# Kernel tuning notes

Hardware: AMD Instinct MI355X
Metric: run time of the kernel (lower is better)

Reference implementation:

```python
import jax, jax.numpy as jnp
import numpy as np

N_NODES = 50000
N_EDGES = 800000
IN_DIM = 128
HID = 128
BN_EPS = 1e-5


def _linear_init(key, fan_in, fan_out):
    kw, kb = jax.random.split(key)
    bound = 1.0 / np.sqrt(fan_in)
    w = jax.random.uniform(kw, (fan_in, fan_out), minval=-bound, maxval=bound, dtype=jnp.float32)
    b = jax.random.uniform(kb, (fan_out,), minval=-bound, maxval=bound, dtype=jnp.float32)
    return w, b


def setup_inputs() -> dict:
    key = jax.random.key(0)
    ks = jax.random.split(key, 8)
    x = jax.random.normal(ks[0], (N_NODES, IN_DIM), dtype=jnp.float32)
    edge_index = jax.random.randint(ks[1], (2, N_EDGES), 0, N_NODES, dtype=jnp.int32)
    # GIN layer 0 MLP: Linear(IN_DIM,HID) -> ReLU -> Linear(HID,HID)
    w0a, b0a = _linear_init(ks[2], IN_DIM, HID)
    w0b, b0b = _linear_init(ks[3], HID, HID)
    # GIN layer 1 MLP
    w1a, b1a = _linear_init(ks[4], HID, HID)
    w1b, b1b = _linear_init(ks[5], HID, HID)
    # encoder BatchNorm affine params (torch init: gamma=1, beta=0)
    bn_gamma = jnp.ones((HID,), jnp.float32)
    bn_beta = jnp.zeros((HID,), jnp.float32)
    # projection head: Linear(HID,HID) -> BatchNorm -> PReLU -> Dropout
    pw, pb = _linear_init(ks[6], HID, HID)
    pbn_gamma = jnp.ones((HID,), jnp.float32)
    pbn_beta = jnp.zeros((HID,), jnp.float32)
    prelu_a = jnp.asarray(0.25, jnp.float32)  # torch PReLU default init
    return {
        'x': x, 'edge_index': edge_index,
        'w0a': w0a, 'b0a': b0a, 'w0b': w0b, 'b0b': b0b,
        'w1a': w1a, 'b1a': b1a, 'w1b': w1b, 'b1b': b1b,
        'bn_gamma': bn_gamma, 'bn_beta': bn_beta,
        'pw': pw, 'pb': pb, 'pbn_gamma': pbn_gamma, 'pbn_beta': pbn_beta,
        'prelu_a': prelu_a,
    }


def _batch_norm(x, gamma, beta):
    # training-mode BatchNorm1d: biased variance over the node (batch) dim
    mu = jnp.mean(x, axis=0)
    var = jnp.var(x, axis=0)
    return gamma * (x - mu) * jax.lax.rsqrt(var + BN_EPS) + beta


def _gin_conv(z, src, dst, wa, ba, wb, bb):
    # sum-aggregate neighbor features: out[i] = (1+eps)*z[i] + sum_{j->i} z[j], eps=0
    agg = jax.ops.segment_sum(z[src], dst, num_segments=N_NODES)
    h = z + agg
    h = jax.nn.relu(h @ wa + ba)
    return h @ wb + bb


def reference(x, edge_index, w0a, b0a, w0b, b0b, w1a, b1a, w1b, b1b,
              bn_gamma, bn_beta, pw, pb, pbn_gamma, pbn_beta, prelu_a):
    src, dst = edge_index[0], edge_index[1]
    z = x
    z = jax.nn.relu(_gin_conv(z, src, dst, w0a, b0a, w0b, b0b))  # dropout: identity (deterministic)
    z = jax.nn.relu(_gin_conv(z, src, dst, w1a, b1a, w1b, b1b))
    z = _batch_norm(z, bn_gamma, bn_beta)
    p = z @ pw + pb
    p = _batch_norm(p, pbn_gamma, pbn_beta)
    p = jnp.where(p > 0, p, prelu_a * p)  # PReLU, single shared parameter
    return z, p
```

## Files before the change

kernel.cpp:

```cpp
#include <hip/hip_runtime.h>
#include <hip/hip_bf16.h>

#define NN 50000
#define NE 800000
#define HD 128
#define BN_EPS 1e-5f
#define MSTR 132
#define NBUK 782
#define PB 200
#define CHUNK 4000

typedef __attribute__((ext_vector_type(8))) __bf16 bf16x8;
typedef __attribute__((ext_vector_type(4))) __bf16 bf16x4;
typedef __attribute__((ext_vector_type(4))) float floatx4;

__global__ __launch_bounds__(256) void k_cast(const float* __restrict__ X,
                                              __bf16* __restrict__ Y,
                                              int* __restrict__ gbtot) {
    const int t = blockIdx.x * 256 + threadIdx.x;
    if (t < 800) gbtot[t] = 0;
    const int i8 = t * 8;
    const float4 a = *(const float4*)&X[i8];
    const float4 b = *(const float4*)&X[i8 + 4];
    bf16x8 o;
    o[0] = (__bf16)a.x; o[1] = (__bf16)a.y; o[2] = (__bf16)a.z; o[3] = (__bf16)a.w;
    o[4] = (__bf16)b.x; o[5] = (__bf16)b.y; o[6] = (__bf16)b.z; o[7] = (__bf16)b.w;
    *(bf16x8*)&Y[i8] = o;
}

__global__ void k_wprep(const float* __restrict__ W0, const float* __restrict__ W1,
                        const float* __restrict__ W2, const float* __restrict__ W3,
                        const float* __restrict__ W4,
                        __bf16* __restrict__ Bh, __bf16* __restrict__ Bl) {
    const int n = blockIdx.x, m = blockIdx.y, k = threadIdx.x;
    const float* W = (m == 0) ? W0 : (m == 1) ? W1 : (m == 2) ? W2 : (m == 3) ? W3 : W4;
    const float w = W[k * HD + n];
    const __bf16 h = (__bf16)w;
    const int ct = n >> 4, lm = n & 15;
    const int ks = k >> 5, lq = (k & 31) >> 3, j = k & 7;
    const int lane = lq * 16 + lm;
    const size_t o = (size_t)m * HD * HD + (size_t)(((ct * 4 + ks) * 64) + lane) * 8 + j;
    Bh[o] = h;
    Bl[o] = (__bf16)(w - (float)h);
}

__global__ __launch_bounds__(256) void k_bcount(const int* __restrict__ dst,
                                                int* __restrict__ gbtot) {
    __shared__ int h[NBUK];
    for (int i = threadIdx.x; i < NBUK; i += 256) h[i] = 0;
    __syncthreads();
    const int e0 = blockIdx.x * CHUNK;
    for (int i = threadIdx.x; i < CHUNK; i += 256)
        atomicAdd(&h[dst[e0 + i] >> 6], 1);
    __syncthreads();
    for (int i = threadIdx.x; i < NBUK; i += 256) {
        const int v = h[i];
        if (v) atomicAdd(&gbtot[i], v);
    }
}

__global__ __launch_bounds__(256) void k_bscan(const int* __restrict__ gbtot,
                                               int* __restrict__ bbase,
                                               int* __restrict__ gcur,
                                               int* __restrict__ rowptr) {
    __shared__ int sh[256];
    const int t = threadIdx.x;
    int v[4];
    int s = 0;
#pragma unroll
    for (int j = 0; j < 4; ++j) {
        const int idx = t * 4 + j;
        v[j] = (idx < NBUK) ? gbtot[idx] : 0;
        s += v[j];
    }
    sh[t] = s;
    __syncthreads();
#pragma unroll
    for (int st = 1; st < 256; st <<= 1) {
        int add = (t >= st) ? sh[t - st] : 0;
        __syncthreads();
        sh[t] += add;
        __syncthreads();
    }
    int run = sh[t] - s;
#pragma unroll
    for (int j = 0; j < 4; ++j) {
        const int idx = t * 4 + j;
        if (idx < NBUK) { bbase[idx] = run; gcur[idx] = run; }
        run += v[j];
    }
    if (t == 255) bbase[NBUK] = run;
    if (t == 0) rowptr[NN] = NE;
}

__global__ __launch_bounds__(256) void k_bscatter(const int* __restrict__ src,
                                                  const int* __restrict__ dst,
                                                  int* __restrict__ gcur,
                                                  int2* __restrict__ pairs) {
    __shared__ int h[NBUK];
    __shared__ int cur[NBUK];
    for (int i = threadIdx.x; i < NBUK; i += 256) h[i] = 0;
    __syncthreads();
    const int e0 = blockIdx.x * CHUNK;
    for (int i = threadIdx.x; i < CHUNK; i += 256)
        atomicAdd(&h[dst[e0 + i] >> 6], 1);
    __syncthreads();
    for (int i = threadIdx.x; i < NBUK; i += 256) {
        const int v = h[i];
        if (v) cur[i] = atomicAdd(&gcur[i], v);
    }
    __syncthreads();
    for (int i = threadIdx.x; i < CHUNK; i += 256) {
        const int d = dst[e0 + i];
        const int pos = atomicAdd(&cur[d >> 6], 1);
        pairs[pos] = make_int2(src[e0 + i], d);
    }
}

__global__ __launch_bounds__(256) void k_csrfin(const int2* __restrict__ pairs,
                                                const int* __restrict__ bbase,
                                                int* __restrict__ rowptr,
                                                int* __restrict__ esrc) {
    __shared__ int cnt[64], lof[64], cur[64];
    const int b = blockIdx.x;
    const int s = bbase[b], e = bbase[b + 1];
    const int tid = threadIdx.x;
    if (tid < 64) cnt[tid] = 0;
    __syncthreads();
    for (int i = s + tid; i < e; i += 256)
        atomicAdd(&cnt[pairs[i].y & 63], 1);
    __syncthreads();
    if (tid == 0) {
        int r = 0;
#pragma unroll
        for (int j = 0; j < 64; ++j) { lof[j] = r; cur[j] = r; r += cnt[j]; }
    }
    __syncthreads();
    if (tid < 64) {
        const int node = b * 64 + tid;
        if (node < NN) rowptr[node] = s + lof[tid];
    }
    for (int i = s + tid; i < e; i += 256) {
        const int2 p = pairs[i];
        const int pos = atomicAdd(&cur[p.y & 63], 1);
        esrc[s + pos] = p.x;
    }
}

__device__ __forceinline__ void split8(const float4 a, const float4 b,
                                       bf16x8& hi, bf16x8& lo) {
    hi[0] = (__bf16)a.x; lo[0] = (__bf16)(a.x - (float)hi[0]);
    hi[1] = (__bf16)a.y; lo[1] = (__bf16)(a.y - (float)hi[1]);
    hi[2] = (__bf16)a.z; lo[2] = (__bf16)(a.z - (float)hi[2]);
    hi[3] = (__bf16)a.w; lo[3] = (__bf16)(a.w - (float)hi[3]);
    hi[4] = (__bf16)b.x; lo[4] = (__bf16)(b.x - (float)hi[4]);
    hi[5] = (__bf16)b.y; lo[5] = (__bf16)(b.y - (float)hi[5]);
    hi[6] = (__bf16)b.z; lo[6] = (__bf16)(b.z - (float)hi[6]);
    hi[7] = (__bf16)b.w; lo[7] = (__bf16)(b.w - (float)hi[7]);
}

__device__ __forceinline__ void addb8(float4& a, float4& b, const bf16x8 v) {
    a.x += (float)v[0]; a.y += (float)v[1]; a.z += (float)v[2]; a.w += (float)v[3];
    b.x += (float)v[4]; b.y += (float)v[5]; b.z += (float)v[6]; b.w += (float)v[7];
}

__global__ __launch_bounds__(256) void k_aggb(const __bf16* __restrict__ Z,
                                              const int* __restrict__ rowptr,
                                              const int* __restrict__ esrc,
                                              float* __restrict__ H) {
    const int g = threadIdx.x >> 4;
    const int lg = threadIdx.x & 15;
    const int node = blockIdx.x * 16 + g;
    const int cb = lg * 8;
    const int start = rowptr[node], end = rowptr[node + 1];
    float4 a = {0.f, 0.f, 0.f, 0.f}, b = {0.f, 0.f, 0.f, 0.f};
    addb8(a, b, *(const bf16x8*)&Z[(size_t)node * HD + cb]);
    int k = start;
    for (; k + 8 <= end; k += 8) {
        const int s0 = esrc[k + 0], s1 = esrc[k + 1];
        const int s2 = esrc[k + 2], s3 = esrc[k + 3];
        const int s4 = esrc[k + 4], s5 = esrc[k + 5];
        const int s6 = esrc[k + 6], s7 = esrc[k + 7];
        const bf16x8 v0 = *(const bf16x8*)&Z[(size_t)s0 * HD + cb];
        const bf16x8 v1 = *(const bf16x8*)&Z[(size_t)s1 * HD + cb];
        const bf16x8 v2 = *(const bf16x8*)&Z[(size_t)s2 * HD + cb];
        const bf16x8 v3 = *(const bf16x8*)&Z[(size_t)s3 * HD + cb];
        const bf16x8 v4 = *(const bf16x8*)&Z[(size_t)s4 * HD + cb];
        const bf16x8 v5 = *(const bf16x8*)&Z[(size_t)s5 * HD + cb];
        const bf16x8 v6 = *(const bf16x8*)&Z[(size_t)s6 * HD + cb];
        const bf16x8 v7 = *(const bf16x8*)&Z[(size_t)s7 * HD + cb];
        addb8(a, b, v0); addb8(a, b, v1); addb8(a, b, v2); addb8(a, b, v3);
        addb8(a, b, v4); addb8(a, b, v5); addb8(a, b, v6); addb8(a, b, v7);
    }
    for (; k + 4 <= end; k += 4) {
        const int s0 = esrc[k + 0], s1 = esrc[k + 1];
        const int s2 = esrc[k + 2], s3 = esrc[k + 3];
        const bf16x8 v0 = *(const bf16x8*)&Z[(size_t)s0 * HD + cb];
        const bf16x8 v1 = *(const bf16x8*)&Z[(size_t)s1 * HD + cb];
        const bf16x8 v2 = *(const bf16x8*)&Z[(size_t)s2 * HD + cb];
        const bf16x8 v3 = *(const bf16x8*)&Z[(size_t)s3 * HD + cb];
        addb8(a, b, v0); addb8(a, b, v1); addb8(a, b, v2); addb8(a, b, v3);
    }
    for (; k < end; ++k) {
        const int s = esrc[k];
        addb8(a, b, *(const bf16x8*)&Z[(size_t)s * HD + cb]);
    }
    *(float4*)&H[(size_t)node * HD + cb] = a;
    *(float4*)&H[(size_t)node * HD + cb + 4] = b;
}

__device__ __forceinline__ void mfma_pass(floatx4 (&acc)[8], const bf16x8 ah,
                                          const bf16x8 al, const __bf16* Bh,
                                          const __bf16* Bl, int ks, int lane) {
    bf16x8 bh[8], bl[8];
#pragma unroll
    for (int ct = 0; ct < 8; ++ct) {
        const size_t bo = (size_t)(((ct * 4 + ks) * 64) + lane) * 8;
        bh[ct] = *(const bf16x8*)&Bh[bo];
        bl[ct] = *(const bf16x8*)&Bl[bo];
    }
    __builtin_amdgcn_sched_barrier(0);
#pragma unroll
    for (int ct = 0; ct < 8; ++ct) {
        acc[ct] = __builtin_amdgcn_mfma_f32_16x16x32_bf16(al, bh[ct], acc[ct], 0, 0, 0);
        acc[ct] = __builtin_amdgcn_mfma_f32_16x16x32_bf16(ah, bl[ct], acc[ct], 0, 0, 0);
        acc[ct] = __builtin_amdgcn_mfma_f32_16x16x32_bf16(ah, bh[ct], acc[ct], 0, 0, 0);
    }
}

template <int STATS, int OUT16>
__global__ __launch_bounds__(256) void k_mlp(const float* __restrict__ A,
                                             const __bf16* __restrict__ Bh1,
                                             const __bf16* __restrict__ Bl1,
                                             const float* __restrict__ b1,
                                             const __bf16* __restrict__ Bh2,
                                             const __bf16* __restrict__ Bl2,
                                             const float* __restrict__ b2,
                                             float* __restrict__ C,
                                             __bf16* __restrict__ C16,
                                             float* __restrict__ pstat) {
    __shared__ float mid[4][16 * MSTR];
    __shared__ float ssum[128], ssq[128];
    const int tid = threadIdx.x;
    const int wid = tid >> 6, lane = tid & 63;
    const int lq = lane >> 4, lm = lane & 15;
    if (STATS) {
        if (tid < 128) { ssum[tid] = 0.f; ssq[tid] = 0.f; }
        __syncthreads();
    }
    const int rowbase = blockIdx.x * 64 + wid * 16;
    const int r0 = min(rowbase + lm, NN - 1);
    float* m = &mid[wid][0];

    bf16x8 ahv[4], alv[4];
    {
        float4 av[8];
#pragma unroll
        for (int ks = 0; ks < 4; ++ks) {
            const int kk = ks * 32 + lq * 8;
            av[ks * 2 + 0] = *(const float4*)&A[(size_t)r0 * HD + kk];
            av[ks * 2 + 1] = *(const float4*)&A[(size_t)r0 * HD + kk + 4];
        }
#pragma unroll
        for (int ks = 0; ks < 4; ++ks)
            split8(av[ks * 2], av[ks * 2 + 1], ahv[ks], alv[ks]);
    }
    floatx4 acc[8];
#pragma unroll
    for (int j = 0; j < 8; ++j) acc[j] = (floatx4){0.f, 0.f, 0.f, 0.f};
#pragma unroll
    for (int ks = 0; ks < 4; ++ks)
        mfma_pass(acc, ahv[ks], alv[ks], Bh1, Bl1, ks, lane);
#pragma unroll
    for (int ct = 0; ct < 8; ++ct) {
        const int col = ct * 16 + lm;
        const float bcol = b1[col];
#pragma unroll
        for (int r = 0; r < 4; ++r)
            m[(lq * 4 + r) * MSTR + col] = fmaxf(acc[ct][r] + bcol, 0.f);
    }
#pragma unroll
    for (int j = 0; j < 8; ++j) acc[j] = (floatx4){0.f, 0.f, 0.f, 0.f};
#pragma unroll
    for (int ks = 0; ks < 4; ++ks) {
        const int kk = ks * 32 + lq * 8;
        const float4 aa = *(const float4*)&m[lm * MSTR + kk];
        const float4 ab = *(const float4*)&m[lm * MSTR + kk + 4];
        bf16x8 ah, al;
        split8(aa, ab, ah, al);
        mfma_pass(acc, ah, al, Bh2, Bl2, ks, lane);
    }
#pragma unroll
    for (int ct = 0; ct < 8; ++ct) {
        const int col = ct * 16 + lm;
        const float bcol = b2[col];
#pragma unroll
        for (int r = 0; r < 4; ++r)
            m[(lq * 4 + r) * MSTR + col] = fmaxf(acc[ct][r] + bcol, 0.f);
    }
    float s0 = 0.f, s1 = 0.f, s2 = 0.f, s3 = 0.f;
    float q0 = 0.f, q1 = 0.f, q2 = 0.f, q3 = 0.f;
    const int c0 = (lane * 4) & 127;
#pragma unroll
    for (int p = 0; p < 8; ++p) {
        const int idx = p * 256 + lane * 4;
        const int r = idx >> 7;
        const float4 v = *(const float4*)&m[r * MSTR + c0];
        const int row = rowbase + r;
        if (row < NN) {
            if (OUT16) {
                bf16x4 o;
                o[0] = (__bf16)v.x; o[1] = (__bf16)v.y;
                o[2] = (__bf16)v.z; o[3] = (__bf16)v.w;
                *(bf16x4*)&C16[(size_t)row * HD + c0] = o;
            } else {
                *(float4*)&C[(size_t)row * HD + c0] = v;
            }
            if (STATS) {
                s0 += v.x; q0 = fmaf(v.x, v.x, q0);
                s1 += v.y; q1 = fmaf(v.y, v.y, q1);
                s2 += v.z; q2 = fmaf(v.z, v.z, q2);
                s3 += v.w; q3 = fmaf(v.w, v.w, q3);
            }
        }
    }
    if (STATS) {
        s0 += __shfl_xor(s0, 32); q0 += __shfl_xor(q0, 32);
        s1 += __shfl_xor(s1, 32); q1 += __shfl_xor(q1, 32);
        s2 += __shfl_xor(s2, 32); q2 += __shfl_xor(q2, 32);
        s3 += __shfl_xor(s3, 32); q3 += __shfl_xor(q3, 32);
        if (lane < 32) {
            atomicAdd(&ssum[c0 + 0], s0); atomicAdd(&ssq[c0 + 0], q0);
            atomicAdd(&ssum[c0 + 1], s1); atomicAdd(&ssq[c0 + 1], q1);
            atomicAdd(&ssum[c0 + 2], s2); atomicAdd(&ssq[c0 + 2], q2);
            atomicAdd(&ssum[c0 + 3], s3); atomicAdd(&ssq[c0 + 3], q3);
        }
        __syncthreads();
        if (tid < 128) {
            pstat[(size_t)blockIdx.x * 256 + tid] = ssum[tid];
            pstat[(size_t)blockIdx.x * 256 + 128 + tid] = ssq[tid];
        }
    }
}

__global__ __launch_bounds__(256) void k_proj(const float* __restrict__ Z2,
                                              const float* __restrict__ bnsc,
                                              const float* __restrict__ bnsh,
                                              float* __restrict__ Zout,
                                              const __bf16* __restrict__ Bh,
                                              const __bf16* __restrict__ Bl,
                                              const float* __restrict__ bias,
                                              float* __restrict__ C,
                                              float* __restrict__ pstat) {
    __shared__ float tb[4][16 * MSTR];
    __shared__ float ssum[128], ssq[128];
    const int tid = threadIdx.x;
    const int wid = tid >> 6, lane = tid & 63;
    const int lq = lane >> 4, lm = lane & 15;
    if (tid < 128) { ssum[tid] = 0.f; ssq[tid] = 0.f; }
    __syncthreads();
    const int rowbase = blockIdx.x * 64 + wid * 16;
    const int r0 = min(rowbase + lm, NN - 1);
    const bool rowok = (rowbase + lm) < NN;
    float* m = &tb[wid][0];

    bf16x8 ahv[4], alv[4];
#pragma unroll
    for (int ks = 0; ks < 4; ++ks) {
        const int kk = ks * 32 + lq * 8;
        const float4 za = *(const float4*)&Z2[(size_t)r0 * HD + kk];
        const float4 zb = *(const float4*)&Z2[(size_t)r0 * HD + kk + 4];
        const float4 sca = *(const float4*)&bnsc[kk];
        const float4 scb = *(const float4*)&bnsc[kk + 4];
        const float4 sha = *(const float4*)&bnsh[kk];
        const float4 shb = *(const float4*)&bnsh[kk + 4];
        float4 aa, ab;
        aa.x = fmaf(za.x, sca.x, sha.x); aa.y = fmaf(za.y, sca.y, sha.y);
        aa.z = fmaf(za.z, sca.z, sha.z); aa.w = fmaf(za.w, sca.w, sha.w);
        ab.x = fmaf(zb.x, scb.x, shb.x); ab.y = fmaf(zb.y, scb.y, shb.y);
        ab.z = fmaf(zb.z, scb.z, shb.z); ab.w = fmaf(zb.w, scb.w, shb.w);
        if (rowok) {
            *(float4*)&Zout[(size_t)r0 * HD + kk] = aa;
            *(float4*)&Zout[(size_t)r0 * HD + kk + 4] = ab;
        }
        split8(aa, ab, ahv[ks], alv[ks]);
    }
    floatx4 acc[8];
#pragma unroll
    for (int j = 0; j < 8; ++j) acc[j] = (floatx4){0.f, 0.f, 0.f, 0.f};
#pragma unroll
    for (int ks = 0; ks < 4; ++ks)
        mfma_pass(acc, ahv[ks], alv[ks], Bh, Bl, ks, lane);
#pragma unroll
    for (int ct = 0; ct < 8; ++ct) {
        const int col = ct * 16 + lm;
        const float bcol = bias[col];
#pragma unroll
        for (int r = 0; r < 4; ++r)
            m[(lq * 4 + r) * MSTR + col] = acc[ct][r] + bcol;
    }
    float s0 = 0.f, s1 = 0.f, s2 = 0.f, s3 = 0.f;
    float q0 = 0.f, q1 = 0.f, q2 = 0.f, q3 = 0.f;
    const int c0 = (lane * 4) & 127;
#pragma unroll
    for (int p = 0; p < 8; ++p) {
        const int idx = p * 256 + lane * 4;
        const int r = idx >> 7;
        const float4 v = *(const float4*)&m[r * MSTR + c0];
        const int row = rowbase + r;
        if (row < NN) {
            *(float4*)&C[(size_t)row * HD + c0] = v;
            s0 += v.x; q0 = fmaf(v.x, v.x, q0);
            s1 += v.y; q1 = fmaf(v.y, v.y, q1);
            s2 += v.z; q2 = fmaf(v.z, v.z, q2);
            s3 += v.w; q3 = fmaf(v.w, v.w, q3);
        }
    }
    s0 += __shfl_xor(s0, 32); q0 += __shfl_xor(q0, 32);
    s1 += __shfl_xor(s1, 32); q1 += __shfl_xor(q1, 32);
    s2 += __shfl_xor(s2, 32); q2 += __shfl_xor(q2, 32);
    s3 += __shfl_xor(s3, 32); q3 += __shfl_xor(q3, 32);
    if (lane < 32) {
        atomicAdd(&ssum[c0 + 0], s0); atomicAdd(&ssq[c0 + 0], q0);
        atomicAdd(&ssum[c0 + 1], s1); atomicAdd(&ssq[c0 + 1], q1);
        atomicAdd(&ssum[c0 + 2], s2); atomicAdd(&ssq[c0 + 2], q2);
        atomicAdd(&ssum[c0 + 3], s3); atomicAdd(&ssq[c0 + 3], q3);
    }
    __syncthreads();
    if (tid < 128) {
        pstat[(size_t)blockIdx.x * 256 + tid] = ssum[tid];
        pstat[(size_t)blockIdx.x * 256 + 128 + tid] = ssq[tid];
    }
}

__global__ __launch_bounds__(256) void k_sred(const float* __restrict__ ps, int nblk,
                                              float* __restrict__ out) {
    const int j = threadIdx.x;
    float acc = 0.f;
    for (int r = blockIdx.x; r < nblk; r += 64)
        acc += ps[(size_t)r * 256 + j];
    out[blockIdx.x * 256 + j] = acc;
}

__global__ void k_bnfin(const float* __restrict__ pb2,
                        const float* __restrict__ gamma, const float* __restrict__ beta,
                        float* __restrict__ scale, float* __restrict__ shift) {
    const int c = threadIdx.x;
    float s = 0.f, q = 0.f;
    for (int b = 0; b < 64; ++b) {
        s += pb2[b * 256 + c];
        q += pb2[b * 256 + 128 + c];
    }
    const float mean = s * (1.f / NN);
    const float var = q * (1.f / NN) - mean * mean;
    const float sc = gamma[c] * rsqrtf(var + BN_EPS);
    scale[c] = sc;
    shift[c] = beta[c] - mean * sc;
}

__global__ void k_bnapply(const float* __restrict__ X, const float* __restrict__ scale,
                          const float* __restrict__ shift, float* __restrict__ Y,
                          const float* __restrict__ pa) {
    const int i4 = (blockIdx.x * 256 + threadIdx.x) * 4;
    const int c = i4 & 127;
    const float4 sc = *(const float4*)&scale[c];
    const float4 sh = *(const float4*)&shift[c];
    const float4 v = *(const float4*)&X[i4];
    float4 y;
    y.x = fmaf(v.x, sc.x, sh.x);
    y.y = fmaf(v.y, sc.y, sh.y);
    y.z = fmaf(v.z, sc.z, sh.z);
    y.w = fmaf(v.w, sc.w, sh.w);
    const float a = pa[0];
    if (y.x < 0.f) y.x *= a;
    if (y.y < 0.f) y.y *= a;
    if (y.z < 0.f) y.z *= a;
    if (y.w < 0.f) y.w *= a;
    *(float4*)&Y[i4] = y;
}

extern "C" void kernel_launch(void* const* d_in, const int* in_sizes, int n_in,
                              void* d_out, int out_size, void* d_ws, size_t ws_size,
                              hipStream_t stream) {
    const float* x = (const float*)d_in[0];
    const int* ei = (const int*)d_in[1];
    const float* w0a = (const float*)d_in[2];
    const float* b0a = (const float*)d_in[3];
    const float* w0b = (const float*)d_in[4];
    const float* b0b = (const float*)d_in[5];
    const float* w1a = (const float*)d_in[6];
    const float* b1a = (const float*)d_in[7];
    const float* w1b = (const float*)d_in[8];
    const float* b1b = (const float*)d_in[9];
    const float* bng = (const float*)d_in[10];
    const float* bnb = (const float*)d_in[11];
    const float* pw  = (const float*)d_in[12];
    const float* pb  = (const float*)d_in[13];
    const float* pbng = (const float*)d_in[14];
    const float* pbnb = (const float*)d_in[15];
    const float* pa = (const float*)d_in[16];

    float* outZ = (float*)d_out;
    float* outP = outZ + (size_t)NN * HD;

    float* ws = (float*)d_ws;
    float* bufH = ws;
    float* st = bufH + (size_t)NN * HD;
    int* rowptr = (int*)(st + 1024);
    int* esrc = rowptr + NN + 64;
    int* gbtot = esrc + NE;
    int* bbase = gbtot + 800;
    int* gcur = bbase + 800;
    __bf16* wth = (__bf16*)(gcur + 800);
    __bf16* wtl = wth + 5 * HD * HD;
    float* ps1 = (float*)(wtl + 5 * HD * HD);
    float* pb2a = ps1 + 800 * 256;
    float* ps2 = pb2a + 64 * 256;
    float* pb2b = ps2 + 800 * 256;

    __bf16* xb  = (__bf16*)bufH;
    __bf16* z1b = xb + (size_t)NN * HD;
    int2* pairs = (int2*)z1b;
    float* Hbuf = outP;

    const int* srcv = ei;
    const int* dstv = ei + NE;

    const int ELV = (NN * HD) / (256 * 4);
    const int CVB = (NN * HD) / (256 * 8);
    const int GB = (NN + 63) / 64;
    const int AB = NN / 16;

    k_wprep<<<dim3(HD, 5), HD, 0, stream>>>(w0a, w0b, w1a, w1b, pw, wth, wtl);
    k_cast<<<CVB, 256, 0, stream>>>(x, xb, gbtot);

    k_bcount<<<PB, 256, 0, stream>>>(dstv, gbtot);
    k_bscan<<<1, 256, 0, stream>>>(gbtot, bbase, gcur, rowptr);
    k_bscatter<<<PB, 256, 0, stream>>>(srcv, dstv, gcur, pairs);
    k_csrfin<<<NBUK, 256, 0, stream>>>(pairs, bbase, rowptr, esrc);

    k_aggb<<<AB, 256, 0, stream>>>(xb, rowptr, esrc, Hbuf);
    k_mlp<0, 1><<<GB, 256, 0, stream>>>(Hbuf,
                                        wth + 0 * HD * HD, wtl + 0 * HD * HD, b0a,
                                        wth + 1 * HD * HD, wtl + 1 * HD * HD, b0b,
                                        nullptr, z1b, nullptr);

    k_aggb<<<AB, 256, 0, stream>>>(z1b, rowptr, esrc, Hbuf);
    k_mlp<1, 0><<<GB, 256, 0, stream>>>(Hbuf,
                                        wth + 2 * HD * HD, wtl + 2 * HD * HD, b1a,
                                        wth + 3 * HD * HD, wtl + 3 * HD * HD, b1b,
                                        outP, nullptr, ps1);

    k_sred<<<64, 256, 0, stream>>>(ps1, GB, pb2a);
    k_bnfin<<<1, 128, 0, stream>>>(pb2a, bng, bnb, st + 256, st + 384);
    k_proj<<<GB, 256, 0, stream>>>(outP, st + 256, st + 384, outZ,
                                   wth + 4 * HD * HD, wtl + 4 * HD * HD, pb,
                                   outP, ps2);

    k_sred<<<64, 256, 0, stream>>>(ps2, GB, pb2b);
    k_bnfin<<<1, 128, 0, stream>>>(pb2b, pbng, pbnb, st + 768, st + 896);
    k_bnapply<<<ELV, 256, 0, stream>>>(outP, st + 768, st + 896, outP, pa);
}
```

Measured before the change: 323.6 us.

## Merge prep kernels and stage MLP weight tiles through double-buffered LDS

Three setup kernels (weight split, input cast, bucket count) become one launch with block ranges, and a memset takes over zeroing the bucket totals. In the MLP and projection kernels, each k-slice of the hi/lo weight tiles is now loaded cooperatively by the four waves into a double-buffered shared-memory tile, prefetching the next slice while MFMAs run. Before, every wave read the full weight tiles from global memory. The change adds a block barrier per slice and extra LDS use, which may lower occupancy.

```diff
diff --git a/kernel.cpp b/kernel.cpp
--- a/kernel.cpp
+++ b/kernel.cpp
@@ -14,48 +14,53 @@
 typedef __attribute__((ext_vector_type(4))) __bf16 bf16x4;
 typedef __attribute__((ext_vector_type(4))) float floatx4;
 
-__global__ __launch_bounds__(256) void k_cast(const float* __restrict__ X,
+__global__ __launch_bounds__(256) void k_prep(const float* __restrict__ W0,
+                                              const float* __restrict__ W1,
+                                              const float* __restrict__ W2,
+                                              const float* __restrict__ W3,
+                                              const float* __restrict__ W4,
+                                              __bf16* __restrict__ Bh,
+                                              __bf16* __restrict__ Bl,
+                                              const float* __restrict__ X,
                                               __bf16* __restrict__ Y,
+                                              const int* __restrict__ dst,
                                               int* __restrict__ gbtot) {
-    const int t = blockIdx.x * 256 + threadIdx.x;
-    if (t < 800) gbtot[t] = 0;
-    const int i8 = t * 8;
-    const float4 a = *(const float4*)&X[i8];
-    const float4 b = *(const float4*)&X[i8 + 4];
-    bf16x8 o;
-    o[0] = (__bf16)a.x; o[1] = (__bf16)a.y; o[2] = (__bf16)a.z; o[3] = (__bf16)a.w;
-    o[4] = (__bf16)b.x; o[5] = (__bf16)b.y; o[6] = (__bf16)b.z; o[7] = (__bf16)b.w;
-    *(bf16x8*)&Y[i8] = o;
-}
-
-__global__ void k_wprep(const float* __restrict__ W0, const float* __restrict__ W1,
-                        const float* __restrict__ W2, const float* __restrict__ W3,
-                        const float* __restrict__ W4,
-                        __bf16* __restrict__ Bh, __bf16* __restrict__ Bl) {
-    const int n = blockIdx.x, m = blockIdx.y, k = threadIdx.x;
-    const float* W = (m == 0) ? W0 : (m == 1) ? W1 : (m == 2) ? W2 : (m == 3) ? W3 : W4;
-    const float w = W[k * HD + n];
-    const __bf16 h = (__bf16)w;
-    const int ct = n >> 4, lm = n & 15;
-    const int ks = k >> 5, lq = (k & 31) >> 3, j = k & 7;
-    const int lane = lq * 16 + lm;
-    const size_t o = (size_t)m * HD * HD + (size_t)(((ct * 4 + ks) * 64) + lane) * 8 + j;
-    Bh[o] = h;
-    Bl[o] = (__bf16)(w - (float)h);
-}
-
-__global__ __launch_bounds__(256) void k_bcount(const int* __restrict__ dst,
-                                                int* __restrict__ gbtot) {
     __shared__ int h[NBUK];
-    for (int i = threadIdx.x; i < NBUK; i += 256) h[i] = 0;
-    __syncthreads();
-    const int e0 = blockIdx.x * CHUNK;
-    for (int i = threadIdx.x; i < CHUNK; i += 256)
-        atomicAdd(&h[dst[e0 + i] >> 6], 1);
-    __syncthreads();
-    for (int i = threadIdx.x; i < NBUK; i += 256) {
-        const int v = h[i];
-        if (v) atomicAdd(&gbtot[i], v);
+    const int b = blockIdx.x;
+    if (b < 320) {
+        const int t = b * 256 + threadIdx.x;
+        const int m = t >> 14;
+        const int rem = t & 16383;
+        const int n = rem >> 7;
+        const int k = rem & 127;
+        const float* W = (m == 0) ? W0 : (m == 1) ? W1 : (m == 2) ? W2 : (m == 3) ? W3 : W4;
+        const float w = W[k * HD + n];
+        const __bf16 hi = (__bf16)w;
+        const int ct = n >> 4, lm = n & 15;
+        const int ks = k >> 5, lq = (k & 31) >> 3, j = k & 7;
+        const int lane = lq * 16 + lm;
+        const size_t o = (size_t)m * HD * HD + (size_t)(((ct * 4 + ks) * 64) + lane) * 8 + j;
+        Bh[o] = hi;
+        Bl[o] = (__bf16)(w - (float)hi);
+    } else if (b < 320 + 3125) {
+        const int i8 = ((b - 320) * 256 + threadIdx.x) * 8;
+        const float4 a = *(const float4*)&X[i8];
+        const float4 c = *(const float4*)&X[i8 + 4];
+        bf16x8 o;
+        o[0] = (__bf16)a.x; o[1] = (__bf16)a.y; o[2] = (__bf16)a.z; o[3] = (__bf16)a.w;
+        o[4] = (__bf16)c.x; o[5] = (__bf16)c.y; o[6] = (__bf16)c.z; o[7] = (__bf16)c.w;
+        *(bf16x8*)&Y[i8] = o;
+    } else {
+        for (int i = threadIdx.x; i < NBUK; i += 256) h[i] = 0;
+        __syncthreads();
+        const int e0 = (b - (320 + 3125)) * CHUNK;
+        for (int i = threadIdx.x; i < CHUNK; i += 256)
+            atomicAdd(&h[dst[e0 + i] >> 6], 1);
+        __syncthreads();
+        for (int i = threadIdx.x; i < NBUK; i += 256) {
+            const int v = h[i];
+            if (v) atomicAdd(&gbtot[i], v);
+        }
     }
 }
 
@@ -209,15 +214,36 @@
     *(float4*)&H[(size_t)node * HD + cb + 4] = b;
 }
 
-__device__ __forceinline__ void mfma_pass(floatx4 (&acc)[8], const bf16x8 ah,
-                                          const bf16x8 al, const __bf16* Bh,
-                                          const __bf16* Bl, int ks, int lane) {
+struct StageRegs { bf16x8 v[4]; };
+
+__device__ __forceinline__ void stage_load(StageRegs& s, const __bf16* __restrict__ Bh,
+                                           const __bf16* __restrict__ Bl,
+                                           int ks, int wid, int lane) {
+#pragma unroll
+    for (int i = 0; i < 4; ++i) {
+        const int chunk = wid * 4 + i;
+        const int ct = chunk & 7;
+        const __bf16* base = (chunk < 8) ? Bh : Bl;
+        s.v[i] = *(const bf16x8*)&base[(size_t)(((ct * 4 + ks) * 64) + lane) * 8];
+    }
+}
+__device__ __forceinline__ void stage_write(const StageRegs& s, __bf16* Bb,
+                                            int wid, int lane) {
+#pragma unroll
+    for (int i = 0; i < 4; ++i) {
+        const int chunk = wid * 4 + i;
+        *(bf16x8*)&Bb[chunk * 512 + lane * 8] = s.v[i];
+    }
+}
+
+__device__ __forceinline__ void mfma_pass_lds(floatx4 (&acc)[8], const bf16x8 ah,
+                                              const bf16x8 al, const __bf16* Bb,
+                                              int lane) {
     bf16x8 bh[8], bl[8];
 #pragma unroll
     for (int ct = 0; ct < 8; ++ct) {
-        const size_t bo = (size_t)(((ct * 4 + ks) * 64) + lane) * 8;
-        bh[ct] = *(const bf16x8*)&Bh[bo];
-        bl[ct] = *(const bf16x8*)&Bl[bo];
+        bh[ct] = *(const bf16x8*)&Bb[ct * 512 + lane * 8];
+        bl[ct] = *(const bf16x8*)&Bb[(8 + ct) * 512 + lane * 8];
     }
     __builtin_amdgcn_sched_barrier(0);
 #pragma unroll
@@ -240,14 +266,12 @@
                                              __bf16* __restrict__ C16,
                                              float* __restrict__ pstat) {
     __shared__ float mid[4][16 * MSTR];
+    __shared__ __bf16 Bb[2][16 * 512];
     __shared__ float ssum[128], ssq[128];
     const int tid = threadIdx.x;
     const int wid = tid >> 6, lane = tid & 63;
     const int lq = lane >> 4, lm = lane & 15;
-    if (STATS) {
-        if (tid < 128) { ssum[tid] = 0.f; ssq[tid] = 0.f; }
-        __syncthreads();
-    }
+    if (STATS && tid < 128) { ssum[tid] = 0.f; ssq[tid] = 0.f; }
     const int rowbase = blockIdx.x * 64 + wid * 16;
     const int r0 = min(rowbase + lm, NN - 1);
     float* m = &mid[wid][0];
@@ -265,30 +289,47 @@
         for (int ks = 0; ks < 4; ++ks)
             split8(av[ks * 2], av[ks * 2 + 1], ahv[ks], alv[ks]);
     }
+    {
+        StageRegs s;
+        stage_load(s, Bh1, Bl1, 0, wid, lane);
+        stage_write(s, &Bb[0][0], wid, lane);
+    }
+    __syncthreads();
+
     floatx4 acc[8];
 #pragma unroll
     for (int j = 0; j < 8; ++j) acc[j] = (floatx4){0.f, 0.f, 0.f, 0.f};
-#pragma unroll
-    for (int ks = 0; ks < 4; ++ks)
-        mfma_pass(acc, ahv[ks], alv[ks], Bh1, Bl1, ks, lane);
-#pragma unroll
-    for (int ct = 0; ct < 8; ++ct) {
-        const int col = ct * 16 + lm;
-        const float bcol = b1[col];
-#pragma unroll
-        for (int r = 0; r < 4; ++r)
-            m[(lq * 4 + r) * MSTR + col] = fmaxf(acc[ct][r] + bcol, 0.f);
-    }
-#pragma unroll
-    for (int j = 0; j < 8; ++j) acc[j] = (floatx4){0.f, 0.f, 0.f, 0.f};
-#pragma unroll
-    for (int ks = 0; ks < 4; ++ks) {
-        const int kk = ks * 32 + lq * 8;
-        const float4 aa = *(const float4*)&m[lm * MSTR + kk];
-        const float4 ab = *(const float4*)&m[lm * MSTR + kk + 4];
+
+#pragma unroll
+    for (int p = 0; p < 8; ++p) {
+        StageRegs s;
+        if (p < 7) {
+            const int pn = p + 1;
+            stage_load(s, (pn < 4) ? Bh1 : Bh2, (pn < 4) ? Bl1 : Bl2, pn & 3, wid, lane);
+        }
         bf16x8 ah, al;
-        split8(aa, ab, ah, al);
-        mfma_pass(acc, ah, al, Bh2, Bl2, ks, lane);
+        if (p < 4) { ah = ahv[p]; al = alv[p]; }
+        else {
+            const int kk = (p & 3) * 32 + lq * 8;
+            const float4 aa = *(const float4*)&m[lm * MSTR + kk];
+            const float4 ab = *(const float4*)&m[lm * MSTR + kk + 4];
+            split8(aa, ab, ah, al);
+        }
+        mfma_pass_lds(acc, ah, al, &Bb[p & 1][0], lane);
+        if (p == 3) {
+#pragma unroll
+            for (int ct = 0; ct < 8; ++ct) {
+                const int col = ct * 16 + lm;
+                const float bcol = b1[col];
+#pragma unroll
+                for (int r = 0; r < 4; ++r)
+                    m[(lq * 4 + r) * MSTR + col] = fmaxf(acc[ct][r] + bcol, 0.f);
+            }
+#pragma unroll
+            for (int j = 0; j < 8; ++j) acc[j] = (floatx4){0.f, 0.f, 0.f, 0.f};
+        }
+        if (p < 7) stage_write(s, &Bb[(p + 1) & 1][0], wid, lane);
+        __syncthreads();
     }
 #pragma unroll
     for (int ct = 0; ct < 8; ++ct) {
@@ -352,17 +393,19 @@
                                               const float* __restrict__ bias,
                                               float* __restrict__ C,
                                               float* __restrict__ pstat) {
-    __shared__ float tb[4][16 * MSTR];
+    __shared__ union {
+        __bf16 bb[2][16 * 512];
+        float tb[4][16 * MSTR];
+    } u;
     __shared__ float ssum[128], ssq[128];
     const int tid = threadIdx.x;
     const int wid = tid >> 6, lane = tid & 63;
     const int lq = lane >> 4, lm = lane & 15;
     if (tid < 128) { ssum[tid] = 0.f; ssq[tid] = 0.f; }
-    __syncthreads();
     const int rowbase = blockIdx.x * 64 + wid * 16;
     const int r0 = min(rowbase + lm, NN - 1);
     const bool rowok = (rowbase + lm) < NN;
-    float* m = &tb[wid][0];
+    float* m = &u.tb[wid][0];
 
     bf16x8 ahv[4], alv[4];
 #pragma unroll
@@ -385,12 +428,24 @@
         }
         split8(aa, ab, ahv[ks], alv[ks]);
     }
+    {
+        StageRegs s;
+        stage_load(s, Bh, Bl, 0, wid, lane);
+        stage_write(s, &u.bb[0][0], wid, lane);
+    }
+    __syncthreads();
+
     floatx4 acc[8];
 #pragma unroll
     for (int j = 0; j < 8; ++j) acc[j] = (floatx4){0.f, 0.f, 0.f, 0.f};
 #pragma unroll
-    for (int ks = 0; ks < 4; ++ks)
-        mfma_pass(acc, ahv[ks], alv[ks], Bh, Bl, ks, lane);
+    for (int p = 0; p < 4; ++p) {
+        StageRegs s;
+        if (p < 3) stage_load(s, Bh, Bl, p + 1, wid, lane);
+        mfma_pass_lds(acc, ahv[p], alv[p], &u.bb[p & 1][0], lane);
+        if (p < 3) stage_write(s, &u.bb[(p + 1) & 1][0], wid, lane);
+        __syncthreads();
+    }
 #pragma unroll
     for (int ct = 0; ct < 8; ++ct) {
         const int col = ct * 16 + lm;
@@ -527,14 +582,14 @@
     const int* dstv = ei + NE;
 
     const int ELV = (NN * HD) / (256 * 4);
-    const int CVB = (NN * HD) / (256 * 8);
     const int GB = (NN + 63) / 64;
     const int AB = NN / 16;
-
-    k_wprep<<<dim3(HD, 5), HD, 0, stream>>>(w0a, w0b, w1a, w1b, pw, wth, wtl);
-    k_cast<<<CVB, 256, 0, stream>>>(x, xb, gbtot);
-
-    k_bcount<<<PB, 256, 0, stream>>>(dstv, gbtot);
+    const int PREPB = 320 + 3125 + PB;
+
+    hipMemsetAsync(gbtot, 0, 800 * sizeof(int), stream);
+    k_prep<<<PREPB, 256, 0, stream>>>(w0a, w0b, w1a, w1b, pw, wth, wtl,
+                                      x, xb, dstv, gbtot);
+
     k_bscan<<<1, 256, 0, stream>>>(gbtot, bbase, gcur, rowptr);
     k_bscatter<<<PB, 256, 0, stream>>>(srcv, dstv, gcur, pairs);
     k_csrfin<<<NBUK, 256, 0, stream>>>(pairs, bbase, rowptr, esrc);
```

Result: faster. 311.5 us (-3.7%).
